# Kernel optimization log

Measured on AMD Instinct MI355X. Metric: run time of the kernel, lower is better.

The kernel has to match this reference:

```python
import jax, jax.numpy as jnp
import numpy as np

B, T, V, E, H, D, R = 64, 21, 12000, 256, 512, 1024, 36


def setup_inputs() -> dict:
    key = jax.random.key(0)
    ks = jax.random.split(key, 16)
    s = 0.02
    inp = {}
    inp["h0"] = jax.random.normal(ks[0], (B, H), jnp.float32)
    inp["object_proposals"] = jax.random.normal(ks[1], (B, R, D), jnp.float32)
    inp["captions"] = jax.random.randint(ks[2], (B, T), 0, V)
    lens = jax.random.randint(ks[3], (B, 1), 2, T + 1)
    inp["caption_lengths"] = lens.at[0, 0].set(T)  # ensure max decode length = T-1 (static)
    inp["emb_W"] = jax.random.normal(ks[4], (V, E)) * s
    inp["wh_W"] = jax.random.normal(ks[5], (H, E)) * s
    inp["wh_b"] = jnp.zeros((H,), jnp.float32)
    inp["wr_W"] = jax.random.normal(ks[6], (D, E)) * s
    inp["wr_b"] = jnp.zeros((D,), jnp.float32)
    inp["rh_W"] = jax.random.normal(ks[7], (H, D)) * s
    inp["rh_b"] = jnp.zeros((H,), jnp.float32)
    inp["w_W"] = jax.random.normal(ks[8], (1, E)) * s
    inp["w_b"] = jnp.zeros((1,), jnp.float32)
    inp["r_W"] = jax.random.normal(ks[9], (1, D)) * s
    inp["r_b"] = jnp.zeros((1,), jnp.float32)
    inp["lstm_Wih"] = jax.random.normal(ks[10], (4 * H, E + D)) * s
    inp["lstm_Whh"] = jax.random.normal(ks[11], (4 * H, H)) * s
    inp["lstm_bih"] = jnp.zeros((4 * H,), jnp.float32)
    inp["lstm_bhh"] = jnp.zeros((4 * H,), jnp.float32)
    return inp


def _forward(h0, object_proposals, captions, caption_lengths,
             emb_W, wh_W, wh_b, wr_W, wr_b, rh_W, rh_b, w_W, w_b, r_W, r_b,
             lstm_Wih, lstm_Whh, lstm_bih, lstm_bhh):
    Bv, Hh = h0.shape
    Dd = object_proposals.shape[-1]
    Tdec = captions.shape[1] - 1

    # sort batch by caption length, descending (stable)
    lens = caption_lengths[:, 0]
    sort_ind = jnp.argsort(-lens)
    lens_s = lens[sort_ind]
    h0s = h0[sort_ind]
    objs = object_proposals[sort_ind]            # [B,R,D]
    caps = captions[sort_ind]                    # [B,T]
    dec = lens_s - 1                             # decode lengths

    emb = emb_W[caps]                            # [B,T,E]

    # time-invariant vocab-wide projections (the torch loop recomputes these each step)
    P_wh = emb_W @ wh_W.T + wh_b                 # [V,H]
    P_wr = emb_W @ wr_W.T + wr_b                 # [V,D]
    P_w = emb_W @ w_W[0] + w_b[0]                # [V]
    # time-invariant region projections
    rh_all = jnp.einsum('brd,hd->brh', objs, rh_W) + rh_b   # [B,R,H]
    r_lin = jnp.einsum('brd,d->br', objs, r_W[0]) + r_b[0]  # [B,R]
    obj_sum = objs.sum(axis=1)                               # [B,D]
    sumv_wr = jnp.einsum('d,brd->br', P_wr.sum(axis=0), objs)  # sum over vocab of wr, [B,R]

    def step(carry, xs):
        h, c, rf = carry
        t, emb_t = xs                             # emb_t: [B,E]
        mask = (dec > t)[:, None]                 # [B,1] active rows
        x = jnp.concatenate([emb_t, rf], axis=1)  # [B,E+D]
        gates = x @ lstm_Wih.T + lstm_bih + h @ lstm_Whh.T + lstm_bhh
        i, f, g, o = jnp.split(gates, 4, axis=1)  # PyTorch LSTMCell gate order
        i, f, o = jax.nn.sigmoid(i), jax.nn.sigmoid(f), jax.nn.sigmoid(o)
        g = jnp.tanh(g)
        c_new = f * c + i * g
        h_new = o * jnp.tanh(c_new)
        h = jnp.where(mask, h_new, h)
        c = jnp.where(mask, c_new, c)
        # attention: w [B,V], sum_r(wr) [B,V], sum_v(wr) [B,R], r [B,R]
        wt = h @ P_wh.T + P_w                                 # [B,V]
        sumr_wr = obj_sum @ P_wr.T                            # [B,V]
        rvec = jnp.einsum('brh,bh->br', rh_all, h) + r_lin    # [B,R]
        preds = wt + sumr_wr + rvec.sum(axis=1, keepdims=True)
        logits = wt.sum(axis=1, keepdims=True) + sumv_wr + rvec
        ra = jax.nn.softmax(logits, axis=1)                   # [B,R]
        rf_new = jnp.einsum('br,brd->bd', ra, objs)           # [B,D]
        rf = jnp.where(mask, rf_new, rf)
        preds_out = jnp.where(mask, preds, 0.0)
        ra_out = jnp.where(mask, ra, 0.0)
        return (h, c, rf), (preds_out, ra_out)

    init = (h0s, h0s, jnp.zeros((Bv, Dd), h0.dtype))
    xs = (jnp.arange(Tdec), jnp.transpose(emb[:, :Tdec, :], (1, 0, 2)))
    _, (P, A) = jax.lax.scan(step, init, xs)
    predictions = jnp.transpose(P, (1, 0, 2))    # [B,Tdec,V]
    attention = jnp.transpose(A, (1, 0, 2))      # [B,Tdec,R]
    return predictions, attention, caps[:, 1:], dec, sort_ind


def reference(h0, object_proposals, captions, caption_lengths,
              emb_W, wh_W, wh_b, wr_W, wr_b, rh_W, rh_b, w_W, w_b, r_W, r_b,
              lstm_Wih, lstm_Whh, lstm_bih, lstm_bhh):
    return _forward(h0, object_proposals, captions, caption_lengths,
                    emb_W, wh_W, wh_b, wr_W, wr_b, rh_W, rh_b, w_W, w_b, r_W, r_b,
                    lstm_Wih, lstm_Whh, lstm_bih, lstm_bhh)
```

## Files before the change

kernel.cpp:

```cpp
#include <hip/hip_runtime.h>
#include <cstdint>
#include <cstddef>

#define B64 64
#define TDEC 20
#define VV 12000
#define EE 256
#define HH 512
#define DD 1024
#define RR 36

typedef __attribute__((ext_vector_type(8))) short bf16x8;
typedef __attribute__((ext_vector_type(4))) float f32x4;

__device__ __forceinline__ unsigned short f2b(float f) {
    unsigned u = __float_as_uint(f);
    unsigned r = (u + 0x7FFFu + ((u >> 16) & 1u)) >> 16;
    return (unsigned short)r;
}
__device__ __forceinline__ float b2f(unsigned short h) {
    return __uint_as_float(((unsigned)h) << 16);
}

__global__ void k_sort(const int* __restrict__ cap_len,
                       const int* __restrict__ captions,
                       int* __restrict__ sind, int* __restrict__ dec_i,
                       int* __restrict__ caps_s,
                       float* __restrict__ out_dec,
                       float* __restrict__ out_sind,
                       float* __restrict__ out_caps)
{
    int i = threadIdx.x;
    __shared__ int lens[B64];
    lens[i] = cap_len[i];
    __syncthreads();
    int li = lens[i];
    int rank = 0;
    for (int j = 0; j < B64; ++j) {
        int lj = lens[j];
        if (lj > li || (lj == li && j < i)) rank++;
    }
    sind[rank] = i;
    dec_i[rank] = li - 1;
    out_dec[rank] = (float)(li - 1);
    out_sind[rank] = (float)i;
    for (int t = 0; t < 21; ++t) {
        int tok = captions[i * 21 + t];
        caps_s[rank * 21 + t] = tok;
        if (t >= 1) out_caps[rank * 20 + (t - 1)] = (float)tok;
    }
}

__global__ void k_init(const float* __restrict__ h0, const int* __restrict__ sind,
                       unsigned short* __restrict__ xN0, float* __restrict__ cT)
{
    int idx = blockIdx.x * blockDim.x + threadIdx.x;
    const int totX = B64 * 1536;
    if (idx < totX) {
        int b = idx / 1536, k = idx - b * 1536;
        unsigned short v = 0;
        if (k >= 1024) v = f2b(h0[sind[b] * HH + (k - 1024)]);
        xN0[idx] = v;
    } else {
        int j = idx - totX;
        if (j < HH * B64) {
            int hp = j >> 6, b = j & 63;
            cT[j] = h0[sind[b] * HH + hp];
        }
    }
}

__global__ void k_gobjs(const float* __restrict__ objs, const int* __restrict__ sind,
                        unsigned short* __restrict__ objs_b)
{
    size_t idx = (size_t)blockIdx.x * blockDim.x + threadIdx.x;
    const size_t total = (size_t)B64 * RR * DD;
    const size_t stride = (size_t)gridDim.x * blockDim.x;
    for (; idx < total; idx += stride) {
        int b = (int)(idx / (RR * DD));
        int rest = (int)(idx % (RR * DD));
        objs_b[idx] = f2b(objs[(size_t)sind[b] * (RR * DD) + rest]);
    }
}

__global__ void k_gA(const float* __restrict__ embW, const int* __restrict__ caps_s,
                     unsigned short* __restrict__ AembB)
{
    int idx = blockIdx.x * blockDim.x + threadIdx.x;
    if (idx >= TDEC * B64 * EE) return;
    int tb = idx >> 8, e = idx & 255;
    int t = tb >> 6, b = tb & 63;
    int tok = caps_s[b * 21 + t];
    AembB[idx] = f2b(embW[(size_t)tok * EE + e]);
}

__global__ void k_cvt2d(const float* __restrict__ src, int ld, int cols,
                        unsigned short* __restrict__ dst, int total)
{
    int idx = blockIdx.x * blockDim.x + threadIdx.x;
    if (idx >= total) return;
    int row = idx / cols, col = idx - row * cols;
    dst[idx] = f2b(src[(size_t)row * ld + col]);
}

__global__ void k_mkwht(const float* __restrict__ whW, unsigned short* __restrict__ whT)
{
    int idx = blockIdx.x * blockDim.x + threadIdx.x;
    if (idx >= EE * HH) return;
    int e = idx >> 9, k = idx & 511;
    whT[idx] = f2b(whW[(size_t)k * EE + e]);
}

__global__ void k_mkwc(const float* __restrict__ Wih, const float* __restrict__ Whh,
                       unsigned short* __restrict__ Wc)
{
    int idx = blockIdx.x * blockDim.x + threadIdx.x;
    if (idx >= 2048 * 1536) return;
    int m = idx / 1536, k = idx - m * 1536;
    int hp = m >> 2, g = m & 3;
    int ro = g * 512 + hp;
    float v = (k < 1024) ? Wih[(size_t)ro * 1280 + 256 + k]
                         : Whh[(size_t)ro * 512 + (k - 1024)];
    Wc[idx] = f2b(v);
}

__global__ void k_embsum(const float* __restrict__ embW, float* __restrict__ partial)
{
    int e = threadIdx.x;
    int v0 = blockIdx.x * 188;
    int v1 = v0 + 188; if (v1 > VV) v1 = VV;
    float a = 0.0f;
    for (int v = v0; v < v1; ++v) a += embW[(size_t)v * EE + e];
    partial[blockIdx.x * EE + e] = a;
}
__global__ void k_embred(const float* __restrict__ partial, float* __restrict__ emb_sum)
{
    int e = threadIdx.x;
    float a = 0.0f;
    for (int j = 0; j < 64; ++j) a += partial[j * EE + e];
    emb_sum[e] = a;
}

__global__ void k_pwsum(const float* __restrict__ emb_sum, const float* __restrict__ wrW,
                        const float* __restrict__ wr_b, float* __restrict__ pw)
{
    __shared__ float es[EE];
    es[threadIdx.x] = emb_sum[threadIdx.x];
    __syncthreads();
    int d = blockIdx.x * 256 + threadIdx.x;
    float a = 0.0f;
    const float* row = wrW + (size_t)d * EE;
    for (int e = 0; e < EE; ++e) a = fmaf(es[e], row[e], a);
    pw[d] = a + 12000.0f * wr_b[d];
}

__global__ void k_objpre(const unsigned short* __restrict__ objs_b, const float* __restrict__ wrW,
                         const float* __restrict__ wr_b, const float* __restrict__ pw,
                         const float* __restrict__ rW, const float* __restrict__ r_b,
                         float* __restrict__ s_wr, float* __restrict__ srb,
                         float* __restrict__ sumv, float* __restrict__ r_lin)
{
    int b = blockIdx.x, tid = threadIdx.x;
    __shared__ float os[DD];
    __shared__ float red[256];
    const unsigned short* ob = objs_b + (size_t)b * RR * DD;
    for (int d = tid; d < DD; d += 256) {
        float a = 0.0f;
        for (int r = 0; r < RR; ++r) a += b2f(ob[r * DD + d]);
        os[d] = a;
    }
    __syncthreads();
    float a = 0.0f;
    for (int d = 0; d < DD; ++d) a = fmaf(os[d], wrW[(size_t)d * EE + tid], a);
    s_wr[b * EE + tid] = a;
    float p = 0.0f;
    for (int d = tid; d < DD; d += 256) p = fmaf(os[d], wr_b[d], p);
    red[tid] = p;
    __syncthreads();
    for (int s = 128; s > 0; s >>= 1) { if (tid < s) red[tid] += red[tid + s]; __syncthreads(); }
    if (tid == 0) srb[b] = red[0];
    if (tid < RR) {
        const unsigned short* row = ob + (size_t)tid * DD;
        float sv = 0.0f, rl = 0.0f;
        for (int d = 0; d < DD; ++d) { float x = b2f(row[d]); sv = fmaf(pw[d], x, sv); rl = fmaf(rW[d], x, rl); }
        sumv[b * RR + tid] = sv;
        r_lin[b * RR + tid] = rl + r_b[0];
    }
}

__global__ __launch_bounds__(256) void k_bgemm(
    const unsigned short* __restrict__ A, int lda,
    const unsigned short* __restrict__ B, int ldb,
    float* __restrict__ C, int ldc, int K,
    const float* __restrict__ bias1, const float* __restrict__ bias2)
{
    int tid = threadIdx.x;
    int wv = tid >> 6, lane = tid & 63;
    int l15 = lane & 15, lg = lane >> 4;
    int m0 = blockIdx.x * 32 + (wv & 1) * 16;
    int n0 = blockIdx.y * 32 + (wv >> 1) * 16;
    const unsigned short* Ar = A + (size_t)(m0 + l15) * lda + lg * 8;
    const unsigned short* Br = B + (size_t)(n0 + l15) * ldb + lg * 8;
    f32x4 acc0 = {0.f, 0.f, 0.f, 0.f}, acc1 = {0.f, 0.f, 0.f, 0.f};
#pragma unroll 4
    for (int k0 = 0; k0 < K; k0 += 64) {
        bf16x8 a0 = *(const bf16x8*)(Ar + k0);
        bf16x8 b0 = *(const bf16x8*)(Br + k0);
        bf16x8 a1 = *(const bf16x8*)(Ar + k0 + 32);
        bf16x8 b1 = *(const bf16x8*)(Br + k0 + 32);
        acc0 = __builtin_amdgcn_mfma_f32_16x16x32_bf16(a0, b0, acc0, 0, 0, 0);
        acc1 = __builtin_amdgcn_mfma_f32_16x16x32_bf16(a1, b1, acc1, 0, 0, 0);
    }
    int n = n0 + l15;
    float badd = 0.0f;
    if (bias1) badd += bias1[n];
    if (bias2) badd += bias2[n];
#pragma unroll
    for (int r = 0; r < 4; ++r) {
        int m = m0 + 4 * lg + r;
        C[(size_t)m * ldc + n] = acc0[r] + acc1[r] + badd;
    }
}

__global__ __launch_bounds__(256) void k_step1(
    const unsigned short* __restrict__ Wc,
    const unsigned short* __restrict__ xin,
    unsigned short* __restrict__ xout,
    const float* __restrict__ ge,
    float* __restrict__ cT,
    const int* __restrict__ dec_i, int t)
{
    int tid = threadIdx.x;
    int wv = tid >> 6, lane = tid & 63;
    int l15 = lane & 15, lg = lane >> 4;
    int m0 = blockIdx.x * 16;
    int n0 = wv * 16;
    int hp = blockIdx.x * 4 + lg;
    int b  = n0 + l15;
    int dec = dec_i[b];
    const float* geb = ge + ((size_t)t * 64 + b) * 2048;
    float ge0 = geb[hp], ge1 = geb[512 + hp], ge2 = geb[1024 + hp], ge3 = geb[1536 + hp];
    float cold = cT[hp * 64 + b];
    unsigned short hold = xin[(size_t)b * 1536 + 1024 + hp];

    const unsigned short* Ar = Wc + (size_t)(m0 + l15) * 1536 + lg * 8;
    const unsigned short* Br = xin + (size_t)(n0 + l15) * 1536 + lg * 8;
    f32x4 acc0 = {0.f, 0.f, 0.f, 0.f}, acc1 = {0.f, 0.f, 0.f, 0.f};
#pragma unroll 6
    for (int k0 = 0; k0 < 1536; k0 += 64) {
        bf16x8 a0 = *(const bf16x8*)(Ar + k0);
        bf16x8 b0 = *(const bf16x8*)(Br + k0);
        bf16x8 a1 = *(const bf16x8*)(Ar + k0 + 32);
        bf16x8 b1 = *(const bf16x8*)(Br + k0 + 32);
        acc0 = __builtin_amdgcn_mfma_f32_16x16x32_bf16(a0, b0, acc0, 0, 0, 0);
        acc1 = __builtin_amdgcn_mfma_f32_16x16x32_bf16(a1, b1, acc1, 0, 0, 0);
    }
    float gi = acc0[0] + acc1[0] + ge0;
    float gf = acc0[1] + acc1[1] + ge1;
    float gg = acc0[2] + acc1[2] + ge2;
    float go = acc0[3] + acc1[3] + ge3;
    float ii = 1.0f / (1.0f + expf(-gi));
    float ff = 1.0f / (1.0f + expf(-gf));
    float oo = 1.0f / (1.0f + expf(-go));
    float g2 = tanhf(gg);
    float cn = ff * cold + ii * g2;
    float hn = oo * tanhf(cn);
    bool act = dec > t;
    if (act) cT[hp * 64 + b] = cn;
    xout[(size_t)b * 1536 + 1024 + hp] = act ? f2b(hn) : hold;
}

__global__ __launch_bounds__(256) void k_step2(
    const unsigned short* __restrict__ xh,
    const unsigned short* __restrict__ xin,
    const unsigned short* __restrict__ objs_b,
    const float* __restrict__ rh_all,
    const float* __restrict__ sumv, const float* __restrict__ r_lin,
    const unsigned short* __restrict__ whT,
    const float* __restrict__ wh_b, const float* __restrict__ wW, const float* __restrict__ w_b,
    const float* __restrict__ emb_sum,
    const float* __restrict__ s_wr, const float* __restrict__ srb,
    const int* __restrict__ dec_i,
    unsigned short* __restrict__ Gb, float* __restrict__ g0,
    float* __restrict__ attn_out, int t)
{
    int b = blockIdx.x, tid = threadIdx.x;
    __shared__ float hs[HH];
    __shared__ float rpart[RR][4];
    __shared__ float rvec_s[RR];
    __shared__ float ra_s[RR];
    __shared__ float lg_s[RR];
    __shared__ float red1[256], red2[256];
    {
        unsigned v = *(const unsigned*)(xh + (size_t)b * 1536 + 1024 + tid * 2);
        hs[tid * 2]     = __uint_as_float((v & 0xFFFFu) << 16);
        hs[tid * 2 + 1] = __uint_as_float(v & 0xFFFF0000u);
    }
    __syncthreads();
    if (tid < RR * 4) {
        int r = tid >> 2, q = tid & 3;
        const float* rh = rh_all + ((size_t)b * RR + r) * HH + q * 128;
        float a = 0.0f;
        const float* hq = hs + q * 128;
#pragma unroll 4
        for (int k = 0; k < 128; ++k) a = fmaf(rh[k], hq[k], a);
        rpart[r][q] = a;
    }
    float u = 0.0f;
    {
        const unsigned short* wr = whT + (size_t)tid * HH;
#pragma unroll 2
        for (int i = 0; i < 64; ++i) {
            bf16x8 w8 = *(const bf16x8*)(wr + i * 8);
#pragma unroll
            for (int j = 0; j < 8; ++j)
                u = fmaf(__uint_as_float(((unsigned)(unsigned short)w8[j]) << 16), hs[i * 8 + j], u);
        }
    }
    float ut = u + wW[tid];
    float swr = s_wr[b * EE + tid];
    Gb[((size_t)t * B64 + b) * EE + tid] = f2b(ut + swr);
    float p1 = 0.0f;
    p1 = fmaf(hs[tid], wh_b[tid], p1);
    p1 = fmaf(hs[tid + 256], wh_b[tid + 256], p1);
    red1[tid] = p1;
    red2[tid] = ut * emb_sum[tid];
    __syncthreads();
    if (tid < RR) rvec_s[tid] = rpart[tid][0] + rpart[tid][1] + rpart[tid][2] + rpart[tid][3]
                                + r_lin[b * RR + tid];
    for (int s = 128; s > 0; s >>= 1) {
        if (tid < s) { red1[tid] += red1[tid + s]; red2[tid] += red2[tid + s]; }
        __syncthreads();
    }
    if (tid == 0) {
        float hwb = red1[0] + w_b[0];
        float wtsum = red2[0] + 12000.0f * hwb;
        float rvs = 0.0f, mx = -3.4e38f;
        for (int r = 0; r < RR; ++r) {
            float rv = rvec_s[r];
            rvs += rv;
            float lg = wtsum + sumv[b * RR + r] + rv;
            lg_s[r] = lg;
            mx = fmaxf(mx, lg);
        }
        g0[t * B64 + b] = hwb + srb[b] + rvs;
        float ssum = 0.0f;
        for (int r = 0; r < RR; ++r) { float e = expf(lg_s[r] - mx); ra_s[r] = e; ssum += e; }
        float inv = 1.0f / ssum;
        for (int r = 0; r < RR; ++r) ra_s[r] *= inv;
    }
    __syncthreads();
    bool act = dec_i[b] > t;
    if (tid < RR) attn_out[((size_t)b * TDEC + t) * RR + tid] = act ? ra_s[tid] : 0.0f;
    {
        int d0 = tid * 4;
        unsigned short* dst = (unsigned short*)(xh + (size_t)b * 1536 + d0);
        if (act) {
            float a0 = 0.f, a1 = 0.f, a2 = 0.f, a3 = 0.f;
            const unsigned short* ob = objs_b + (size_t)b * RR * DD + d0;
#pragma unroll 4
            for (int r = 0; r < RR; ++r) {
                ushort4 o4 = *(const ushort4*)(ob + (size_t)r * DD);
                a0 = fmaf(ra_s[r], b2f(o4.x), a0);
                a1 = fmaf(ra_s[r], b2f(o4.y), a1);
                a2 = fmaf(ra_s[r], b2f(o4.z), a2);
                a3 = fmaf(ra_s[r], b2f(o4.w), a3);
            }
            ushort4 w4; w4.x = f2b(a0); w4.y = f2b(a1); w4.z = f2b(a2); w4.w = f2b(a3);
            *(ushort4*)dst = w4;
        } else {
            *(ushort4*)dst = *(const ushort4*)(xin + (size_t)b * 1536 + d0);
        }
    }
}

__global__ __launch_bounds__(256) void k_preds(
    const unsigned short* __restrict__ Gb, const unsigned short* __restrict__ embB,
    const float* __restrict__ g0, const int* __restrict__ dec_i,
    float* __restrict__ out)
{
    int tid = threadIdx.x;
    int wv = tid >> 6, lane = tid & 63;
    int l15 = lane & 15, lg = lane >> 4;
    int tq = blockIdx.x;
    int n00 = blockIdx.y * 128;
    int m0 = tq * 64 + wv * 16;
    bf16x8 afr[8];
    const unsigned short* Ar = Gb + (size_t)(m0 + l15) * EE + lg * 8;
#pragma unroll
    for (int k = 0; k < 8; ++k) afr[k] = *(const bf16x8*)(Ar + k * 32);
    float add[4]; bool act[4]; int brow[4];
#pragma unroll
    for (int r = 0; r < 4; ++r) {
        int bb = wv * 16 + 4 * lg + r;
        brow[r] = bb;
        add[r] = g0[tq * 64 + bb];
        act[r] = dec_i[bb] > tq;
    }
    const bf16x8 zb = {0, 0, 0, 0, 0, 0, 0, 0};
#pragma unroll
    for (int nf = 0; nf < 8; ++nf) {
        int nb = n00 + nf * 16 + l15;
        bool bok = nb < VV;
        const unsigned short* Br = embB + (size_t)nb * EE + lg * 8;
        f32x4 acc = {0.f, 0.f, 0.f, 0.f};
#pragma unroll
        for (int k = 0; k < 8; ++k) {
            bf16x8 bb8 = bok ? *(const bf16x8*)(Br + k * 32) : zb;
            acc = __builtin_amdgcn_mfma_f32_16x16x32_bf16(afr[k], bb8, acc, 0, 0, 0);
        }
        if (bok) {
#pragma unroll
            for (int r = 0; r < 4; ++r) {
                float v = act[r] ? acc[r] + add[r] : 0.0f;
                out[((size_t)brow[r] * TDEC + tq) * VV + nb] = v;
            }
        }
    }
}

extern "C" void kernel_launch(void* const* d_in, const int* in_sizes, int n_in,
                              void* d_out, int out_size, void* d_ws, size_t ws_size,
                              hipStream_t stream)
{
    const float* h0      = (const float*)d_in[0];
    const float* objs    = (const float*)d_in[1];
    const int*   caps    = (const int*)d_in[2];
    const int*   cap_len = (const int*)d_in[3];
    const float* embW    = (const float*)d_in[4];
    const float* whW     = (const float*)d_in[5];
    const float* wh_b    = (const float*)d_in[6];
    const float* wrW     = (const float*)d_in[7];
    const float* wr_b    = (const float*)d_in[8];
    const float* rhW     = (const float*)d_in[9];
    const float* rh_b    = (const float*)d_in[10];
    const float* wW      = (const float*)d_in[11];
    const float* w_b     = (const float*)d_in[12];
    const float* rW      = (const float*)d_in[13];
    const float* r_b     = (const float*)d_in[14];
    const float* Wih     = (const float*)d_in[15];
    const float* Whh     = (const float*)d_in[16];
    const float* bih     = (const float*)d_in[17];
    const float* bhh     = (const float*)d_in[18];

    float* out = (float*)d_out;
    float* out_pred = out;
    float* out_attn = out + 15360000;
    float* out_caps = out + 15406080;
    float* out_dec  = out + 15407360;
    float* out_sind = out + 15407424;

    float* f = (float*)d_ws;
    size_t o = 0;
    float* rh_all  = f + o; o += (size_t)B64 * RR * HH;
    float* ge      = f + o; o += (size_t)TDEC * B64 * 2048;
    float* cT      = f + o; o += (size_t)HH * B64;
    float* g0      = f + o; o += TDEC * B64;
    float* embpart = f + o; o += 64 * EE;
    float* emb_sum = f + o; o += EE;
    float* pw      = f + o; o += DD;
    float* sumv    = f + o; o += B64 * RR;
    float* r_lin   = f + o; o += B64 * RR;
    float* s_wr    = f + o; o += B64 * EE;
    float* srb     = f + o; o += B64;
    o = (o + 3) & ~(size_t)3;
    unsigned short* us = (unsigned short*)(f + o);
    size_t uo = 0;
    unsigned short* xN0    = us + uo; uo += (size_t)B64 * 1536;
    unsigned short* xN1    = us + uo; uo += (size_t)B64 * 1536;
    unsigned short* objs_b = us + uo; uo += (size_t)B64 * RR * DD;
    unsigned short* AembB  = us + uo; uo += (size_t)TDEC * B64 * EE;
    unsigned short* rhW_b  = us + uo; uo += (size_t)HH * DD;
    unsigned short* embB   = us + uo; uo += (size_t)VV * EE;
    unsigned short* WihB   = us + uo; uo += (size_t)2048 * EE;
    unsigned short* whT    = us + uo; uo += (size_t)EE * HH;
    unsigned short* Wc     = us + uo; uo += (size_t)2048 * 1536;
    unsigned short* Gb     = us + uo; uo += (size_t)TDEC * B64 * EE;
    int* ibase  = (int*)(us + uo);
    int* sind   = ibase;
    int* dec_i  = ibase + 64;
    int* caps_s = ibase + 128;

    k_sort<<<1, 64, 0, stream>>>(cap_len, caps, sind, dec_i, caps_s, out_dec, out_sind, out_caps);
    k_init<<<512, 256, 0, stream>>>(h0, sind, xN0, cT);
    k_gobjs<<<1024, 256, 0, stream>>>(objs, sind, objs_b);
    k_gA<<<1280, 256, 0, stream>>>(embW, caps_s, AembB);
    k_embsum<<<64, 256, 0, stream>>>(embW, embpart);
    k_embred<<<1, 256, 0, stream>>>(embpart, emb_sum);
    k_pwsum<<<4, 256, 0, stream>>>(emb_sum, wrW, wr_b, pw);
    k_objpre<<<64, 256, 0, stream>>>(objs_b, wrW, wr_b, pw, rW, r_b, s_wr, srb, sumv, r_lin);
    k_cvt2d<<<2048, 256, 0, stream>>>(rhW, DD, DD, rhW_b, HH * DD);
    k_cvt2d<<<12000, 256, 0, stream>>>(embW, EE, EE, embB, VV * EE);
    k_cvt2d<<<2048, 256, 0, stream>>>(Wih, 1280, EE, WihB, 2048 * EE);
    k_mkwht<<<512, 256, 0, stream>>>(whW, whT);
    k_mkwc<<<12288, 256, 0, stream>>>(Wih, Whh, Wc);
    {
        dim3 g1(72, 16);
        k_bgemm<<<g1, 256, 0, stream>>>(objs_b, DD, rhW_b, DD, rh_all, HH, DD, rh_b, nullptr);
        dim3 g2(40, 64);
        k_bgemm<<<g2, 256, 0, stream>>>(AembB, EE, WihB, EE, ge, 2048, EE, bih, bhh);
    }
    for (int t = 0; t < TDEC; ++t) {
        unsigned short* xin  = (t & 1) ? xN1 : xN0;
        unsigned short* xout = (t & 1) ? xN0 : xN1;
        k_step1<<<128, 256, 0, stream>>>(Wc, xin, xout, ge, cT, dec_i, t);
        k_step2<<<64, 256, 0, stream>>>(xout, xin, objs_b, rh_all, sumv, r_lin, whT,
                                        wh_b, wW, w_b, emb_sum, s_wr, srb, dec_i,
                                        Gb, g0, out_attn, t);
    }
    {
        dim3 g3(20, 94);
        k_preds<<<g3, 256, 0, stream>>>(Gb, embB, g0, dec_i, out_pred);
    }
}
```

Measured before the change: 1.085 ms.

## Fuse recurrent steps into persistent cooperative kernel and merge weight prep

Replaces the 40 per-step launches of k_step1/k_step2 with a single cooperative kernel of 64 blocks by 512 threads that loops over time, using grid.sync between the LSTM gate phase and the attention phase. Several weight-conversion kernels are merged into one grid-stride prep kernel. The embedding-sum reduction is split across more blocks. The prediction kernel now stages its output tile in shared memory so it can write coalesced float4 stores. These changes aim to cut launch overhead and improve store coalescing. The cost is grid-wide barriers, and only 64 blocks run the LSTM GEMM on a large GPU.

```diff
diff --git a/kernel.cpp b/kernel.cpp
--- a/kernel.cpp
+++ b/kernel.cpp
@@ -1,6 +1,9 @@
 #include <hip/hip_runtime.h>
+#include <hip/hip_cooperative_groups.h>
 #include <cstdint>
 #include <cstddef>
+
+namespace cg = cooperative_groups;
 
 #define B64 64
 #define TDEC 20
@@ -52,7 +55,7 @@
 }
 
 __global__ void k_init(const float* __restrict__ h0, const int* __restrict__ sind,
-                       unsigned short* __restrict__ xN0, float* __restrict__ cT)
+                       unsigned short* __restrict__ xA, float* __restrict__ cT)
 {
     int idx = blockIdx.x * blockDim.x + threadIdx.x;
     const int totX = B64 * 1536;
@@ -60,7 +63,7 @@
         int b = idx / 1536, k = idx - b * 1536;
         unsigned short v = 0;
         if (k >= 1024) v = f2b(h0[sind[b] * HH + (k - 1024)]);
-        xN0[idx] = v;
+        xA[idx] = v;
     } else {
         int j = idx - totX;
         if (j < HH * B64) {
@@ -73,14 +76,11 @@
 __global__ void k_gobjs(const float* __restrict__ objs, const int* __restrict__ sind,
                         unsigned short* __restrict__ objs_b)
 {
-    size_t idx = (size_t)blockIdx.x * blockDim.x + threadIdx.x;
-    const size_t total = (size_t)B64 * RR * DD;
-    const size_t stride = (size_t)gridDim.x * blockDim.x;
-    for (; idx < total; idx += stride) {
-        int b = (int)(idx / (RR * DD));
-        int rest = (int)(idx % (RR * DD));
-        objs_b[idx] = f2b(objs[(size_t)sind[b] * (RR * DD) + rest]);
-    }
+    int idx = blockIdx.x * blockDim.x + threadIdx.x;
+    if (idx >= B64 * RR * DD) return;
+    int b = idx / (RR * DD);
+    int rest = idx - b * (RR * DD);
+    objs_b[idx] = f2b(objs[(size_t)sind[b] * (RR * DD) + rest]);
 }
 
 __global__ void k_gA(const float* __restrict__ embW, const int* __restrict__ caps_s,
@@ -94,50 +94,60 @@
     AembB[idx] = f2b(embW[(size_t)tok * EE + e]);
 }
 
-__global__ void k_cvt2d(const float* __restrict__ src, int ld, int cols,
-                        unsigned short* __restrict__ dst, int total)
-{
-    int idx = blockIdx.x * blockDim.x + threadIdx.x;
-    if (idx >= total) return;
-    int row = idx / cols, col = idx - row * cols;
-    dst[idx] = f2b(src[(size_t)row * ld + col]);
-}
-
-__global__ void k_mkwht(const float* __restrict__ whW, unsigned short* __restrict__ whT)
-{
-    int idx = blockIdx.x * blockDim.x + threadIdx.x;
-    if (idx >= EE * HH) return;
-    int e = idx >> 9, k = idx & 511;
-    whT[idx] = f2b(whW[(size_t)k * EE + e]);
-}
-
-__global__ void k_mkwc(const float* __restrict__ Wih, const float* __restrict__ Whh,
+#define T_EMB  3072000
+#define T_WIH  524288
+#define T_RH   524288
+#define T_WHT  131072
+#define T_WC   3145728
+#define T_ALL  (T_EMB + T_WIH + T_RH + T_WHT + T_WC)
+__global__ void k_prep(const float* __restrict__ embW, const float* __restrict__ Wih,
+                       const float* __restrict__ Whh, const float* __restrict__ rhW,
+                       const float* __restrict__ whW,
+                       unsigned short* __restrict__ embB, unsigned short* __restrict__ WihB,
+                       unsigned short* __restrict__ rhW_b, unsigned short* __restrict__ whT,
                        unsigned short* __restrict__ Wc)
 {
-    int idx = blockIdx.x * blockDim.x + threadIdx.x;
-    if (idx >= 2048 * 1536) return;
-    int m = idx / 1536, k = idx - m * 1536;
-    int hp = m >> 2, g = m & 3;
-    int ro = g * 512 + hp;
-    float v = (k < 1024) ? Wih[(size_t)ro * 1280 + 256 + k]
-                         : Whh[(size_t)ro * 512 + (k - 1024)];
-    Wc[idx] = f2b(v);
+    for (int idx = blockIdx.x * blockDim.x + threadIdx.x; idx < T_ALL;
+         idx += gridDim.x * blockDim.x) {
+        int i = idx;
+        if (i < T_EMB) { embB[i] = f2b(embW[i]); continue; }
+        i -= T_EMB;
+        if (i < T_WIH) {
+            int row = i >> 8, col = i & 255;
+            WihB[i] = f2b(Wih[(size_t)row * 1280 + col]);
+            continue;
+        }
+        i -= T_WIH;
+        if (i < T_RH) { rhW_b[i] = f2b(rhW[i]); continue; }
+        i -= T_RH;
+        if (i < T_WHT) {
+            int e = i >> 9, k = i & 511;
+            whT[i] = f2b(whW[(size_t)k * EE + e]);
+            continue;
+        }
+        i -= T_WHT;
+        int m = i / 1536, k = i - m * 1536;
+        int hp = m >> 2, g = m & 3;
+        int ro = g * 512 + hp;
+        float v = (k < 1024) ? Wih[(size_t)ro * 1280 + 256 + k]
+                             : Whh[(size_t)ro * 512 + (k - 1024)];
+        Wc[i] = f2b(v);
+    }
 }
 
 __global__ void k_embsum(const float* __restrict__ embW, float* __restrict__ partial)
 {
     int e = threadIdx.x;
-    int v0 = blockIdx.x * 188;
-    int v1 = v0 + 188; if (v1 > VV) v1 = VV;
+    int v0 = blockIdx.x * 50;
     float a = 0.0f;
-    for (int v = v0; v < v1; ++v) a += embW[(size_t)v * EE + e];
+    for (int v = v0; v < v0 + 50; ++v) a += embW[(size_t)v * EE + e];
     partial[blockIdx.x * EE + e] = a;
 }
 __global__ void k_embred(const float* __restrict__ partial, float* __restrict__ emb_sum)
 {
     int e = threadIdx.x;
     float a = 0.0f;
-    for (int j = 0; j < 64; ++j) a += partial[j * EE + e];
+    for (int j = 0; j < 240; ++j) a += partial[j * EE + e];
     emb_sum[e] = a;
 }
 
@@ -222,57 +232,11 @@
     }
 }
 
-__global__ __launch_bounds__(256) void k_step1(
+__global__ __launch_bounds__(512) void k_recur(
     const unsigned short* __restrict__ Wc,
-    const unsigned short* __restrict__ xin,
-    unsigned short* __restrict__ xout,
-    const float* __restrict__ ge,
-    float* __restrict__ cT,
-    const int* __restrict__ dec_i, int t)
-{
-    int tid = threadIdx.x;
-    int wv = tid >> 6, lane = tid & 63;
-    int l15 = lane & 15, lg = lane >> 4;
-    int m0 = blockIdx.x * 16;
-    int n0 = wv * 16;
-    int hp = blockIdx.x * 4 + lg;
-    int b  = n0 + l15;
-    int dec = dec_i[b];
-    const float* geb = ge + ((size_t)t * 64 + b) * 2048;
-    float ge0 = geb[hp], ge1 = geb[512 + hp], ge2 = geb[1024 + hp], ge3 = geb[1536 + hp];
-    float cold = cT[hp * 64 + b];
-    unsigned short hold = xin[(size_t)b * 1536 + 1024 + hp];
-
-    const unsigned short* Ar = Wc + (size_t)(m0 + l15) * 1536 + lg * 8;
-    const unsigned short* Br = xin + (size_t)(n0 + l15) * 1536 + lg * 8;
-    f32x4 acc0 = {0.f, 0.f, 0.f, 0.f}, acc1 = {0.f, 0.f, 0.f, 0.f};
-#pragma unroll 6
-    for (int k0 = 0; k0 < 1536; k0 += 64) {
-        bf16x8 a0 = *(const bf16x8*)(Ar + k0);
-        bf16x8 b0 = *(const bf16x8*)(Br + k0);
-        bf16x8 a1 = *(const bf16x8*)(Ar + k0 + 32);
-        bf16x8 b1 = *(const bf16x8*)(Br + k0 + 32);
-        acc0 = __builtin_amdgcn_mfma_f32_16x16x32_bf16(a0, b0, acc0, 0, 0, 0);
-        acc1 = __builtin_amdgcn_mfma_f32_16x16x32_bf16(a1, b1, acc1, 0, 0, 0);
-    }
-    float gi = acc0[0] + acc1[0] + ge0;
-    float gf = acc0[1] + acc1[1] + ge1;
-    float gg = acc0[2] + acc1[2] + ge2;
-    float go = acc0[3] + acc1[3] + ge3;
-    float ii = 1.0f / (1.0f + expf(-gi));
-    float ff = 1.0f / (1.0f + expf(-gf));
-    float oo = 1.0f / (1.0f + expf(-go));
-    float g2 = tanhf(gg);
-    float cn = ff * cold + ii * g2;
-    float hn = oo * tanhf(cn);
-    bool act = dec > t;
-    if (act) cT[hp * 64 + b] = cn;
-    xout[(size_t)b * 1536 + 1024 + hp] = act ? f2b(hn) : hold;
-}
-
-__global__ __launch_bounds__(256) void k_step2(
-    const unsigned short* __restrict__ xh,
-    const unsigned short* __restrict__ xin,
+    unsigned short* __restrict__ xA, unsigned short* __restrict__ xB,
+    const float* __restrict__ ge, float* __restrict__ cT,
+    const int* __restrict__ dec_i,
     const unsigned short* __restrict__ objs_b,
     const float* __restrict__ rh_all,
     const float* __restrict__ sumv, const float* __restrict__ r_lin,
@@ -280,97 +244,154 @@
     const float* __restrict__ wh_b, const float* __restrict__ wW, const float* __restrict__ w_b,
     const float* __restrict__ emb_sum,
     const float* __restrict__ s_wr, const float* __restrict__ srb,
-    const int* __restrict__ dec_i,
     unsigned short* __restrict__ Gb, float* __restrict__ g0,
-    float* __restrict__ attn_out, int t)
-{
-    int b = blockIdx.x, tid = threadIdx.x;
+    float* __restrict__ attn_out)
+{
+    cg::grid_group grid = cg::this_grid();
+    const int tid = threadIdx.x;
+    const int blk = blockIdx.x;
+    const int wv = tid >> 6, lane = tid & 63;
+    const int l15 = lane & 15, lg = lane >> 4;
+    const int tileid = blk * 8 + wv;
+    const int m0 = (tileid >> 2) * 16;
+    const int n0 = (tileid & 3) * 16;
+    const int hp1 = (m0 >> 2) + lg;
+    const int b1 = n0 + l15;
+    const int dec1 = dec_i[b1];
+    const int b2 = blk;
+    const int dec2 = dec_i[b2];
+
     __shared__ float hs[HH];
-    __shared__ float rpart[RR][4];
+    __shared__ float rpart[RR][8];
     __shared__ float rvec_s[RR];
     __shared__ float ra_s[RR];
-    __shared__ float lg_s[RR];
-    __shared__ float red1[256], red2[256];
-    {
-        unsigned v = *(const unsigned*)(xh + (size_t)b * 1536 + 1024 + tid * 2);
-        hs[tid * 2]     = __uint_as_float((v & 0xFFFFu) << 16);
-        hs[tid * 2 + 1] = __uint_as_float(v & 0xFFFF0000u);
-    }
-    __syncthreads();
-    if (tid < RR * 4) {
-        int r = tid >> 2, q = tid & 3;
-        const float* rh = rh_all + ((size_t)b * RR + r) * HH + q * 128;
-        float a = 0.0f;
-        const float* hq = hs + q * 128;
+    __shared__ float red1[512];
+    __shared__ float red2[256];
+    __shared__ float up[256][2];
+
+    for (int t = 0; t < TDEC; ++t) {
+        const unsigned short* xin = (t & 1) ? xB : xA;
+        unsigned short* xout = (t & 1) ? xA : xB;
+
+        {
+            const unsigned short* Ar = Wc + (size_t)(m0 + l15) * 1536 + lg * 8;
+            const unsigned short* Br = xin + (size_t)(n0 + l15) * 1536 + lg * 8;
+            f32x4 acc0 = {0.f, 0.f, 0.f, 0.f}, acc1 = {0.f, 0.f, 0.f, 0.f};
+#pragma unroll 6
+            for (int k0 = 0; k0 < 1536; k0 += 64) {
+                bf16x8 a0 = *(const bf16x8*)(Ar + k0);
+                bf16x8 bb0 = *(const bf16x8*)(Br + k0);
+                bf16x8 a1 = *(const bf16x8*)(Ar + k0 + 32);
+                bf16x8 bb1 = *(const bf16x8*)(Br + k0 + 32);
+                acc0 = __builtin_amdgcn_mfma_f32_16x16x32_bf16(a0, bb0, acc0, 0, 0, 0);
+                acc1 = __builtin_amdgcn_mfma_f32_16x16x32_bf16(a1, bb1, acc1, 0, 0, 0);
+            }
+            const float* geb = ge + ((size_t)t * B64 + b1) * 2048;
+            float gi = acc0[0] + acc1[0] + geb[hp1];
+            float gf = acc0[1] + acc1[1] + geb[512 + hp1];
+            float gg = acc0[2] + acc1[2] + geb[1024 + hp1];
+            float go = acc0[3] + acc1[3] + geb[1536 + hp1];
+            float ii = 1.0f / (1.0f + expf(-gi));
+            float ff = 1.0f / (1.0f + expf(-gf));
+            float oo = 1.0f / (1.0f + expf(-go));
+            float g2 = tanhf(gg);
+            float cold = cT[hp1 * 64 + b1];
+            float cn = ff * cold + ii * g2;
+            float hn = oo * tanhf(cn);
+            unsigned short hold = xin[(size_t)b1 * 1536 + 1024 + hp1];
+            bool act = dec1 > t;
+            if (act) cT[hp1 * 64 + b1] = cn;
+            xout[(size_t)b1 * 1536 + 1024 + hp1] = act ? f2b(hn) : hold;
+        }
+        grid.sync();
+
+        {
+            float hv = b2f(xout[(size_t)b2 * 1536 + 1024 + tid]);
+            hs[tid] = hv;
+            red1[tid] = hv * wh_b[tid];
+            __syncthreads();
+            {
+                int e = tid & 255, hf = tid >> 8;
+                const unsigned short* wr = whT + (size_t)e * HH + hf * 256;
+                const float* hq = hs + hf * 256;
+                float u = 0.0f;
 #pragma unroll 4
-        for (int k = 0; k < 128; ++k) a = fmaf(rh[k], hq[k], a);
-        rpart[r][q] = a;
-    }
-    float u = 0.0f;
-    {
-        const unsigned short* wr = whT + (size_t)tid * HH;
-#pragma unroll 2
-        for (int i = 0; i < 64; ++i) {
-            bf16x8 w8 = *(const bf16x8*)(wr + i * 8);
-#pragma unroll
-            for (int j = 0; j < 8; ++j)
-                u = fmaf(__uint_as_float(((unsigned)(unsigned short)w8[j]) << 16), hs[i * 8 + j], u);
-        }
-    }
-    float ut = u + wW[tid];
-    float swr = s_wr[b * EE + tid];
-    Gb[((size_t)t * B64 + b) * EE + tid] = f2b(ut + swr);
-    float p1 = 0.0f;
-    p1 = fmaf(hs[tid], wh_b[tid], p1);
-    p1 = fmaf(hs[tid + 256], wh_b[tid + 256], p1);
-    red1[tid] = p1;
-    red2[tid] = ut * emb_sum[tid];
-    __syncthreads();
-    if (tid < RR) rvec_s[tid] = rpart[tid][0] + rpart[tid][1] + rpart[tid][2] + rpart[tid][3]
-                                + r_lin[b * RR + tid];
-    for (int s = 128; s > 0; s >>= 1) {
-        if (tid < s) { red1[tid] += red1[tid + s]; red2[tid] += red2[tid + s]; }
-        __syncthreads();
-    }
-    if (tid == 0) {
-        float hwb = red1[0] + w_b[0];
-        float wtsum = red2[0] + 12000.0f * hwb;
-        float rvs = 0.0f, mx = -3.4e38f;
-        for (int r = 0; r < RR; ++r) {
-            float rv = rvec_s[r];
-            rvs += rv;
-            float lg = wtsum + sumv[b * RR + r] + rv;
-            lg_s[r] = lg;
-            mx = fmaxf(mx, lg);
-        }
-        g0[t * B64 + b] = hwb + srb[b] + rvs;
-        float ssum = 0.0f;
-        for (int r = 0; r < RR; ++r) { float e = expf(lg_s[r] - mx); ra_s[r] = e; ssum += e; }
-        float inv = 1.0f / ssum;
-        for (int r = 0; r < RR; ++r) ra_s[r] *= inv;
-    }
-    __syncthreads();
-    bool act = dec_i[b] > t;
-    if (tid < RR) attn_out[((size_t)b * TDEC + t) * RR + tid] = act ? ra_s[tid] : 0.0f;
-    {
-        int d0 = tid * 4;
-        unsigned short* dst = (unsigned short*)(xh + (size_t)b * 1536 + d0);
-        if (act) {
-            float a0 = 0.f, a1 = 0.f, a2 = 0.f, a3 = 0.f;
-            const unsigned short* ob = objs_b + (size_t)b * RR * DD + d0;
+                for (int i = 0; i < 32; ++i) {
+                    bf16x8 w8 = *(const bf16x8*)(wr + i * 8);
+#pragma unroll
+                    for (int j = 0; j < 8; ++j)
+                        u = fmaf(b2f((unsigned short)w8[j]), hq[i * 8 + j], u);
+                }
+                up[e][hf] = u;
+            }
+            if (tid < RR * 8) {
+                int r = tid >> 3, q = tid & 7;
+                const float* rh = rh_all + ((size_t)b2 * RR + r) * HH + q * 64;
+                const float* hq = hs + q * 64;
+                float a = 0.0f;
 #pragma unroll 4
-            for (int r = 0; r < RR; ++r) {
-                ushort4 o4 = *(const ushort4*)(ob + (size_t)r * DD);
-                a0 = fmaf(ra_s[r], b2f(o4.x), a0);
-                a1 = fmaf(ra_s[r], b2f(o4.y), a1);
-                a2 = fmaf(ra_s[r], b2f(o4.z), a2);
-                a3 = fmaf(ra_s[r], b2f(o4.w), a3);
-            }
-            ushort4 w4; w4.x = f2b(a0); w4.y = f2b(a1); w4.z = f2b(a2); w4.w = f2b(a3);
-            *(ushort4*)dst = w4;
-        } else {
-            *(ushort4*)dst = *(const ushort4*)(xin + (size_t)b * 1536 + d0);
-        }
+                for (int k = 0; k < 64; ++k) a = fmaf(rh[k], hq[k], a);
+                rpart[r][q] = a;
+            }
+            __syncthreads();
+            float ut = 0.0f;
+            if (tid < 256) {
+                ut = up[tid][0] + up[tid][1] + wW[tid];
+                Gb[((size_t)t * B64 + b2) * EE + tid] = f2b(ut + s_wr[b2 * EE + tid]);
+                red2[tid] = ut * emb_sum[tid];
+            }
+            if (tid < RR) {
+                float a = rpart[tid][0] + rpart[tid][1] + rpart[tid][2] + rpart[tid][3]
+                        + rpart[tid][4] + rpart[tid][5] + rpart[tid][6] + rpart[tid][7];
+                rvec_s[tid] = a + r_lin[b2 * RR + tid];
+            }
+            __syncthreads();
+            for (int s = 256; s > 0; s >>= 1) {
+                if (tid < s) {
+                    red1[tid] += red1[tid + s];
+                    if (s <= 128) red2[tid] += red2[tid + s];
+                }
+                __syncthreads();
+            }
+            if (tid < 64) {
+                float hwb = red1[0] + w_b[0];
+                float wtsum = red2[0] + 12000.0f * hwb;
+                float rv = (tid < RR) ? rvec_s[tid] : 0.0f;
+                float lgv = (tid < RR) ? (wtsum + sumv[b2 * RR + tid] + rv) : -3.0e38f;
+                float mx = lgv;
+#pragma unroll
+                for (int o = 32; o > 0; o >>= 1) mx = fmaxf(mx, __shfl_xor(mx, o));
+                float ev = (tid < RR) ? __expf(lgv - mx) : 0.0f;
+                float sm = ev, rvs = rv;
+#pragma unroll
+                for (int o = 32; o > 0; o >>= 1) { sm += __shfl_xor(sm, o); rvs += __shfl_xor(rvs, o); }
+                if (tid < RR) ra_s[tid] = ev / sm;
+                if (tid == 0) g0[t * B64 + b2] = hwb + srb[b2] + rvs;
+            }
+            __syncthreads();
+            bool act = dec2 > t;
+            if (tid < RR) attn_out[((size_t)b2 * TDEC + t) * RR + tid] = act ? ra_s[tid] : 0.0f;
+            {
+                int d0 = tid * 2;
+                unsigned short* dst = xout + (size_t)b2 * 1536 + d0;
+                if (act) {
+                    float a0 = 0.f, a1 = 0.f;
+                    const unsigned short* ob = objs_b + (size_t)b2 * (RR * DD) + d0;
+#pragma unroll 4
+                    for (int r = 0; r < RR; ++r) {
+                        ushort2 o2 = *(const ushort2*)(ob + r * DD);
+                        float w = ra_s[r];
+                        a0 = fmaf(w, b2f(o2.x), a0);
+                        a1 = fmaf(w, b2f(o2.y), a1);
+                    }
+                    ushort2 w2; w2.x = f2b(a0); w2.y = f2b(a1);
+                    *(ushort2*)dst = w2;
+                } else {
+                    *(ushort2*)dst = *(const ushort2*)(xin + (size_t)b2 * 1536 + d0);
+                }
+            }
+        }
+        grid.sync();
     }
 }
 
@@ -379,24 +400,20 @@
     const float* __restrict__ g0, const int* __restrict__ dec_i,
     float* __restrict__ out)
 {
+    __shared__ float outs[64 * 132];
+    __shared__ float sadd[64];
+    __shared__ int sact[64];
     int tid = threadIdx.x;
     int wv = tid >> 6, lane = tid & 63;
     int l15 = lane & 15, lg = lane >> 4;
     int tq = blockIdx.x;
     int n00 = blockIdx.y * 128;
-    int m0 = tq * 64 + wv * 16;
+    int m0w = wv * 16;
+    if (tid < 64) { sadd[tid] = g0[tq * 64 + tid]; sact[tid] = dec_i[tid] > tq; }
     bf16x8 afr[8];
-    const unsigned short* Ar = Gb + (size_t)(m0 + l15) * EE + lg * 8;
+    const unsigned short* Ar = Gb + (size_t)(tq * 64 + m0w + l15) * EE + lg * 8;
 #pragma unroll
     for (int k = 0; k < 8; ++k) afr[k] = *(const bf16x8*)(Ar + k * 32);
-    float add[4]; bool act[4]; int brow[4];
-#pragma unroll
-    for (int r = 0; r < 4; ++r) {
-        int bb = wv * 16 + 4 * lg + r;
-        brow[r] = bb;
-        add[r] = g0[tq * 64 + bb];
-        act[r] = dec_i[bb] > tq;
-    }
     const bf16x8 zb = {0, 0, 0, 0, 0, 0, 0, 0};
 #pragma unroll
     for (int nf = 0; nf < 8; ++nf) {
@@ -409,12 +426,25 @@
             bf16x8 bb8 = bok ? *(const bf16x8*)(Br + k * 32) : zb;
             acc = __builtin_amdgcn_mfma_f32_16x16x32_bf16(afr[k], bb8, acc, 0, 0, 0);
         }
-        if (bok) {
-#pragma unroll
-            for (int r = 0; r < 4; ++r) {
-                float v = act[r] ? acc[r] + add[r] : 0.0f;
-                out[((size_t)brow[r] * TDEC + tq) * VV + nb] = v;
-            }
+#pragma unroll
+        for (int r = 0; r < 4; ++r)
+            outs[(m0w + 4 * lg + r) * 132 + nf * 16 + l15] = acc[r];
+    }
+    __syncthreads();
+#pragma unroll
+    for (int it = 0; it < 8; ++it) {
+        int row = it * 8 + (tid >> 5);
+        int c = (tid & 31) * 4;
+        if (n00 + c < VV) {
+            float add = sadd[row];
+            bool a = sact[row] != 0;
+            const float* src = outs + row * 132 + c;
+            float4 v;
+            v.x = a ? src[0] + add : 0.0f;
+            v.y = a ? src[1] + add : 0.0f;
+            v.z = a ? src[2] + add : 0.0f;
+            v.w = a ? src[3] + add : 0.0f;
+            *(float4*)(out + ((size_t)row * TDEC + tq) * VV + n00 + c) = v;
         }
     }
 }
@@ -456,7 +486,7 @@
     float* ge      = f + o; o += (size_t)TDEC * B64 * 2048;
     float* cT      = f + o; o += (size_t)HH * B64;
     float* g0      = f + o; o += TDEC * B64;
-    float* embpart = f + o; o += 64 * EE;
+    float* embpart = f + o; o += 240 * EE;
     float* emb_sum = f + o; o += EE;
     float* pw      = f + o; o += DD;
     float* sumv    = f + o; o += B64 * RR;
@@ -466,8 +496,8 @@
     o = (o + 3) & ~(size_t)3;
     unsigned short* us = (unsigned short*)(f + o);
     size_t uo = 0;
-    unsigned short* xN0    = us + uo; uo += (size_t)B64 * 1536;
-    unsigned short* xN1    = us + uo; uo += (size_t)B64 * 1536;
+    unsigned short* xA     = us + uo; uo += (size_t)B64 * 1536;
+    unsigned short* xB     = us + uo; uo += (size_t)B64 * 1536;
     unsigned short* objs_b = us + uo; uo += (size_t)B64 * RR * DD;
     unsigned short* AembB  = us + uo; uo += (size_t)TDEC * B64 * EE;
     unsigned short* rhW_b  = us + uo; uo += (size_t)HH * DD;
@@ -482,31 +512,28 @@
     int* caps_s = ibase + 128;
 
     k_sort<<<1, 64, 0, stream>>>(cap_len, caps, sind, dec_i, caps_s, out_dec, out_sind, out_caps);
-    k_init<<<512, 256, 0, stream>>>(h0, sind, xN0, cT);
-    k_gobjs<<<1024, 256, 0, stream>>>(objs, sind, objs_b);
+    k_init<<<512, 256, 0, stream>>>(h0, sind, xA, cT);
+    k_gobjs<<<9216, 256, 0, stream>>>(objs, sind, objs_b);
     k_gA<<<1280, 256, 0, stream>>>(embW, caps_s, AembB);
-    k_embsum<<<64, 256, 0, stream>>>(embW, embpart);
+    k_prep<<<8192, 256, 0, stream>>>(embW, Wih, Whh, rhW, whW, embB, WihB, rhW_b, whT, Wc);
+    k_embsum<<<240, 256, 0, stream>>>(embW, embpart);
     k_embred<<<1, 256, 0, stream>>>(embpart, emb_sum);
     k_pwsum<<<4, 256, 0, stream>>>(emb_sum, wrW, wr_b, pw);
     k_objpre<<<64, 256, 0, stream>>>(objs_b, wrW, wr_b, pw, rW, r_b, s_wr, srb, sumv, r_lin);
-    k_cvt2d<<<2048, 256, 0, stream>>>(rhW, DD, DD, rhW_b, HH * DD);
-    k_cvt2d<<<12000, 256, 0, stream>>>(embW, EE, EE, embB, VV * EE);
-    k_cvt2d<<<2048, 256, 0, stream>>>(Wih, 1280, EE, WihB, 2048 * EE);
-    k_mkwht<<<512, 256, 0, stream>>>(whW, whT);
-    k_mkwc<<<12288, 256, 0, stream>>>(Wih, Whh, Wc);
     {
         dim3 g1(72, 16);
         k_bgemm<<<g1, 256, 0, stream>>>(objs_b, DD, rhW_b, DD, rh_all, HH, DD, rh_b, nullptr);
         dim3 g2(40, 64);
         k_bgemm<<<g2, 256, 0, stream>>>(AembB, EE, WihB, EE, ge, 2048, EE, bih, bhh);
     }
-    for (int t = 0; t < TDEC; ++t) {
-        unsigned short* xin  = (t & 1) ? xN1 : xN0;
-        unsigned short* xout = (t & 1) ? xN0 : xN1;
-        k_step1<<<128, 256, 0, stream>>>(Wc, xin, xout, ge, cT, dec_i, t);
-        k_step2<<<64, 256, 0, stream>>>(xout, xin, objs_b, rh_all, sumv, r_lin, whT,
-                                        wh_b, wW, w_b, emb_sum, s_wr, srb, dec_i,
-                                        Gb, g0, out_attn, t);
+    {
+        void* args[] = {
+            (void*)&Wc, (void*)&xA, (void*)&xB, (void*)&ge, (void*)&cT, (void*)&dec_i,
+            (void*)&objs_b, (void*)&rh_all, (void*)&sumv, (void*)&r_lin, (void*)&whT,
+            (void*)&wh_b, (void*)&wW, (void*)&w_b, (void*)&emb_sum, (void*)&s_wr,
+            (void*)&srb, (void*)&Gb, (void*)&g0, (void*)&out_attn
+        };
+        hipLaunchCooperativeKernel((const void*)k_recur, dim3(64), dim3(512), args, 0, stream);
     }
     {
         dim3 g3(20, 94);
```

Result: slower. 1.479 ms (+36.4%).
